# Kernel tuning notes

Measured on AMD Instinct MI355X. Metric: run time of the kernel, lower is better.

The kernel has to match this reference:

```python
import jax, jax.numpy as jnp
import numpy as np

B, S, H = 2, 4096, 2048
NH, NKV, HD = 16, 4, 128          # heads, kv heads, head_dim = H // NH
GS_RATIO = 0.25                    # hardcoded in MyAttention.forward
ROPE_BASE = 10000.0


def rotate_half(x):
    h = x.shape[-1] // 2
    return jnp.concatenate((-x[..., h:], x[..., :h]), axis=-1)


def setup_inputs() -> dict:
    key = jax.random.key(0)
    ks = jax.random.split(key, 5)
    g = int(S * GS_RATIO)
    hidden_states = jax.random.normal(ks[0], (B, S, H), jnp.float32)
    position_ids = jnp.tile(jnp.arange(S, dtype=jnp.int32)[None, :], (B, 1))
    # causal additive mask per group window (0 keep, -1e9 masked)
    i = jnp.arange(g)
    causal = i[None, :] <= i[:, None]
    attention_mask = jnp.broadcast_to(
        jnp.where(causal, 0.0, -1e9).astype(jnp.float32)[None, None], (B, 1, g, g)
    )
    sc = 0.02
    Wq = (jax.random.normal(ks[1], (H, NH * HD), jnp.float32) * sc)
    Wk = (jax.random.normal(ks[2], (H, NKV * HD), jnp.float32) * sc)
    Wv = (jax.random.normal(ks[3], (H, NKV * HD), jnp.float32) * sc)
    Wo = (jax.random.normal(ks[4], (NH * HD, H), jnp.float32) * sc)
    return {"hidden_states": hidden_states, "attention_mask": attention_mask,
            "position_ids": position_ids, "Wq": Wq, "Wk": Wk, "Wv": Wv, "Wo": Wo}


def reference(hidden_states, attention_mask, position_ids, Wq, Wk, Wv, Wo):
    B_, S_, H_ = hidden_states.shape
    g = int(S_ * GS_RATIO)
    ng = S_ // g
    n_rep = NH // NKV

    # QKV projections -> (B, heads, S, HD)
    q = (hidden_states @ Wq).reshape(B_, S_, NH, HD).transpose(0, 2, 1, 3)
    k = (hidden_states @ Wk).reshape(B_, S_, NKV, HD).transpose(0, 2, 1, 3)
    v = (hidden_states @ Wv).reshape(B_, S_, NKV, HD).transpose(0, 2, 1, 3)

    # RoPE
    inv_freq = 1.0 / (ROPE_BASE ** (jnp.arange(0, HD, 2, dtype=jnp.float32) / HD))
    t = jnp.arange(S_, dtype=jnp.float32)
    emb = jnp.concatenate([jnp.outer(t, inv_freq)] * 2, axis=-1)  # (S, HD)
    cos = jnp.cos(emb)[position_ids][:, None]  # (B,1,S,HD)
    sin = jnp.sin(emb)[position_ids][:, None]
    q = q * cos + rotate_half(q) * sin
    k = k * cos + rotate_half(k) * sin

    # GQA repeat_kv
    k = jnp.repeat(k, n_rep, axis=1)
    v = jnp.repeat(v, n_rep, axis=1)

    # S2-Attn shift: roll second half of heads by -g/2 along seq, then group
    def shift(x):
        x = jnp.concatenate([x[:, :NH // 2],
                             jnp.roll(x[:, NH // 2:], -g // 2, axis=2)], axis=1)
        return x.transpose(0, 2, 1, 3).reshape(B_ * ng, g, NH, HD).transpose(0, 2, 1, 3)

    q, k, v = shift(q), shift(k), shift(v)

    attn = jnp.einsum('bhqd,bhkd->bhqk', q, k) / np.float32(np.sqrt(HD))
    mask = jnp.tile(attention_mask, (ng, 1, 1, 1))  # (B*ng,1,g,g)
    attn = attn + mask
    attn = jax.nn.softmax(attn.astype(jnp.float32), axis=-1).astype(q.dtype)

    out = jnp.einsum('bhqk,bhkd->bhqd', attn, v)  # (B*ng, NH, g, HD)
    out = out.transpose(0, 2, 1, 3).reshape(B_, S_, NH, HD)
    # undo shift for second half of heads (+g/2 along seq)
    out = jnp.concatenate([out[:, :, :NH // 2],
                           jnp.roll(out[:, :, NH // 2:], g // 2, axis=1)], axis=2)
    out = out.reshape(B_, S_, NH * HD) @ Wo
    return out
```

## Files before the change

kernel.cpp:

```cpp
#include <hip/hip_runtime.h>
#include <math.h>

typedef unsigned short u16;
typedef short bf16x8 __attribute__((ext_vector_type(8)));
typedef float f32x4 __attribute__((ext_vector_type(4)));


__device__ __forceinline__ u16 f2bf(float x) {
  union { float f; unsigned u; } c; c.f = x;
  unsigned r = (c.u + 0x7FFFu + ((c.u >> 16) & 1u)) >> 16;
  return (u16)r;
}
__device__ __forceinline__ float bf2f(u16 x) {
  union { unsigned u; float f; } c; c.u = ((unsigned)x) << 16;
  return c.f;
}

#define GLD16(gp, lp)                                                   \
  __builtin_amdgcn_global_load_lds(                                     \
      (__attribute__((address_space(1))) void*)(gp),                    \
      (__attribute__((address_space(3))) void*)(lp), 16, 0, 0)

__global__ __launch_bounds__(256) void cast_bf16_vec(
    const float* __restrict__ X, u16* __restrict__ Y) {
  const size_t i = ((size_t)blockIdx.x * 256 + threadIdx.x) * 4;
  float4 v = *(const float4*)(X + i);
  ushort4 o;
  o.x = f2bf(v.x); o.y = f2bf(v.y); o.z = f2bf(v.z); o.w = f2bf(v.w);
  *(ushort4*)(Y + i) = o;
}

__global__ __launch_bounds__(256) void wt_cast(
    const float* __restrict__ W, u16* __restrict__ Wt, int K, int N) {
  const int bk = blockIdx.y * 64;
  const int bn = blockIdx.x * 64;
  __shared__ float T[64 * 65];
  const int tid = threadIdx.x;
  #pragma unroll
  for (int u = 0; u < 16; ++u) {
    int idx = tid + u * 256;
    int kl = idx >> 6, nl = idx & 63;
    T[kl * 65 + nl] = W[(size_t)(bk + kl) * N + bn + nl];
  }
  __syncthreads();
  #pragma unroll
  for (int u = 0; u < 16; ++u) {
    int idx = tid + u * 256;
    int nl = idx >> 6, kl = idx & 63;
    Wt[(size_t)(bn + nl) * K + bk + kl] = f2bf(T[kl * 65 + nl]);
  }
}

__global__ __launch_bounds__(512) void gemm_bf16_256(
    const u16* __restrict__ A, const u16* __restrict__ Bt,
    float* __restrict__ Cf, u16* __restrict__ Cb, int M, int N, int K) {
  __shared__ u16 As[4][256 * 32];
  __shared__ u16 Bs[4][256 * 32];

  const int tid = threadIdx.x;

  const int gridN = N >> 8;
  const int nwg = gridDim.x * gridDim.y;
  const int orig = blockIdx.y * gridDim.x + blockIdx.x;
  const int q8 = nwg >> 3, r8 = nwg & 7;
  const int xcd = orig & 7, lid = orig >> 3;
  const int wgid = (xcd < r8 ? xcd * (q8 + 1) : r8 * (q8 + 1) + (xcd - r8) * q8) + lid;
  const int bm = (wgid / gridN) << 8;
  const int bn = (wgid % gridN) << 8;

  const int w = tid >> 6, lane = tid & 63;
  const int col = lane & 15, quad = lane >> 4;
  const int wm = w >> 2, wn = w & 3;
  const int sw = (col >> 1) & 3;

  const int srow = tid >> 2;
  const int scp  = tid & 3;
  const int sc   = scp ^ ((srow >> 1) & 3);

  const u16* Ag = A  + (size_t)bm * K;
  const u16* Bg = Bt + (size_t)bn * K;
  const u16* aS0 = Ag + (size_t)srow * K + sc * 8;
  const u16* aS1 = Ag + (size_t)(srow + 128) * K + sc * 8;
  const u16* bS0 = Bg + (size_t)srow * K + sc * 8;
  const u16* bS1 = Bg + (size_t)(srow + 128) * K + sc * 8;
  const int ldst0 = srow * 32 + scp * 8;
  const int ldst1 = (srow + 128) * 32 + scp * 8;

#define STAGE_A(t, buf) { GLD16(aS0 + (size_t)(t) * 32, &As[buf][ldst0]); \
                          GLD16(aS1 + (size_t)(t) * 32, &As[buf][ldst1]); }
#define STAGE_B(t, buf) { GLD16(bS0 + (size_t)(t) * 32, &Bs[buf][ldst0]); \
                          GLD16(bS1 + (size_t)(t) * 32, &Bs[buf][ldst1]); }

  f32x4 acc[8][4];
  #pragma unroll
  for (int i = 0; i < 8; ++i)
    #pragma unroll
    for (int j = 0; j < 4; ++j) acc[i][j] = (f32x4)(0.0f);

  const int NT = K >> 5;

  STAGE_A(0, 0); STAGE_B(0, 0);
  if (NT > 1) {
    STAGE_A(1, 1); STAGE_B(1, 1);
    asm volatile("s_waitcnt vmcnt(4)" ::: "memory");
  } else {
    asm volatile("s_waitcnt vmcnt(0)" ::: "memory");
  }
  __builtin_amdgcn_s_barrier();
  asm volatile("" ::: "memory");

  const int aoff = (wm * 128 + col) * 32 + (quad ^ sw) * 8;
  const int boff = (wn * 64  + col) * 32 + (quad ^ sw) * 8;

  for (int t = 0; t < NT; ++t) {
    const int cur = t & 3;
    const bool pf = (t + 2 < NT);
    const int pbuf = (t + 2) & 3;

    bf16x8 af[4], bfr[4];
    #pragma unroll
    for (int i = 0; i < 4; ++i)
      af[i] = *(const bf16x8*)&As[cur][aoff + (16 * i) * 32];
    #pragma unroll
    for (int j = 0; j < 4; ++j)
      bfr[j] = *(const bf16x8*)&Bs[cur][boff + (16 * j) * 32];
    if (pf) STAGE_A(t + 2, pbuf);
    __builtin_amdgcn_s_barrier();
    asm volatile("s_waitcnt lgkmcnt(0)");
    __builtin_amdgcn_s_setprio(1);
    #pragma unroll
    for (int i = 0; i < 4; ++i)
      #pragma unroll
      for (int j = 0; j < 4; ++j)
        acc[i][j] = __builtin_amdgcn_mfma_f32_16x16x32_bf16(af[i], bfr[j], acc[i][j], 0, 0, 0);
    __builtin_amdgcn_s_setprio(0);
    __builtin_amdgcn_s_barrier();

    bf16x8 af2[4];
    #pragma unroll
    for (int i = 0; i < 4; ++i)
      af2[i] = *(const bf16x8*)&As[cur][aoff + ((64 + 16 * i)) * 32];
    if (pf) STAGE_B(t + 2, pbuf);
    __builtin_amdgcn_s_barrier();
    asm volatile("s_waitcnt lgkmcnt(0)");
    __builtin_amdgcn_s_setprio(1);
    #pragma unroll
    for (int i = 0; i < 4; ++i)
      #pragma unroll
      for (int j = 0; j < 4; ++j)
        acc[4 + i][j] = __builtin_amdgcn_mfma_f32_16x16x32_bf16(af2[i], bfr[j], acc[4 + i][j], 0, 0, 0);
    __builtin_amdgcn_s_setprio(0);

    if (pf) asm volatile("s_waitcnt vmcnt(4)" ::: "memory");
    else    asm volatile("s_waitcnt vmcnt(0)" ::: "memory");
    __builtin_amdgcn_s_barrier();
    asm volatile("" ::: "memory");
  }

  const int crow0 = bm + wm * 128 + quad * 4;
  const int ccol0 = bn + wn * 64 + col;
  #pragma unroll
  for (int i = 0; i < 8; ++i) {
    const int row0 = crow0 + 16 * i;
    #pragma unroll
    for (int j = 0; j < 4; ++j) {
      const int cc = ccol0 + 16 * j;
      #pragma unroll
      for (int r = 0; r < 4; ++r) {
        if (Cb) Cb[(size_t)(row0 + r) * N + cc] = f2bf(acc[i][j][r]);
        else    Cf[(size_t)(row0 + r) * N + cc] = acc[i][j][r];
      }
    }
  }
#undef STAGE_A
#undef STAGE_B
}

__global__ __launch_bounds__(256) void rope_qkv(
    u16* __restrict__ QKV, const int* __restrict__ pos) {
  const unsigned idx = blockIdx.x * 256 + threadIdx.x;
  const int d = idx & 63;
  const unsigned rest = idx >> 6;
  const int hh = rest % 20;
  const unsigned bs = rest / 20;

  const int colbase = (hh < 16) ? hh * 128 : 2048 + (hh - 16) * 128;
  u16* p = QKV + (size_t)bs * 3072 + colbase + d;
  const float x0 = bf2f(p[0]);
  const float x1 = bf2f(p[64]);
  const float t = (float)pos[bs];
  const float inv_freq = __expf((float)d * -0.14391156509676332f);
  float s, c;
  __sincosf(t * inv_freq, &s, &c);
  const float sc = (hh < 16) ? 0.08838834764831845f : 1.0f;
  p[0]  = f2bf((x0 * c - x1 * s) * sc);
  p[64] = f2bf((x1 * c + x0 * s) * sc);
}

__global__ __launch_bounds__(256) void v_transpose(
    const u16* __restrict__ QKV, u16* __restrict__ Vt) {
  const int bid = blockIdx.x;
  const int st = bid & 63;
  const int kvh = (bid >> 6) & 3;
  const int b = bid >> 8;
  __shared__ u16 T[64 * 136];
  const int tid = threadIdx.x;
  #pragma unroll
  for (int u = 0; u < 4; ++u) {
    int idx = tid + u * 256;
    int sl = idx >> 4, ch = idx & 15;
    *(uint4*)&T[sl * 136 + ch * 8] =
        *(const uint4*)(QKV + ((size_t)(b * 4096 + st * 64 + sl)) * 3072 + 2560 + kvh * 128 + ch * 8);
  }
  __syncthreads();
  #pragma unroll
  for (int u = 0; u < 32; ++u) {
    int idx = tid + u * 256;
    int d = idx >> 6, sl = idx & 63;
    Vt[((size_t)((b * 4 + kvh) * 128 + d)) * 4096 + st * 64 + sl] = T[sl * 136 + d];
  }
}

__global__ __launch_bounds__(256) void attn_mfma(
    const u16* __restrict__ QKV, const u16* __restrict__ Vt,
    u16* __restrict__ Ob) {
  __shared__ u16 Ks[64 * 136];
  __shared__ u16 Vs[128 * 72];
  __shared__ u16 Ps[4][16 * 72];

  const int bid = blockIdx.x;
  const int qt = 15 - (bid & 15);
  const int h  = (bid >> 4) & 15;
  const int gi = (bid >> 8) & 3;
  const int b  = bid >> 10;

  const int tid = threadIdx.x;
  const int w = tid >> 6, lane = tid & 63;
  const int col = lane & 15, quad = lane >> 4;

  const int shift = (h >= 8) ? 512 : 0;
  const int base_s = gi * 1024;
  const int kvh = h >> 2;

  const int sq0 = (base_s + qt * 64 + shift) & 4095;
  {
    const u16* qsrc = QKV + ((size_t)(b * 4096 + sq0)) * 3072 + h * 128;
    #pragma unroll
    for (int u = 0; u < 4; ++u) {
      int idx = tid + u * 256;
      int row = idx >> 4, ch = idx & 15;
      *(uint4*)&Ks[row * 136 + ch * 8] =
          *(const uint4*)(qsrc + (size_t)row * 3072 + ch * 8);
    }
  }
  __syncthreads();
  bf16x8 aq[4];
  #pragma unroll
  for (int kk = 0; kk < 4; ++kk)
    aq[kk] = *(const bf16x8*)&Ks[(w * 16 + col) * 136 + kk * 32 + quad * 8];

  f32x4 o[8];
  #pragma unroll
  for (int jd = 0; jd < 8; ++jd) o[jd] = (f32x4)(0.0f);
  float lp[4] = {0.0f, 0.0f, 0.0f, 0.0f};

  u16* Pw = &Ps[w][0];
  const int qrow_l = w * 16 + quad * 4;

  for (int kt = 0; kt <= qt; ++kt) {
    const int sk0 = (base_s + kt * 64 + shift) & 4095;
    __syncthreads();
    {
      const u16* ksrc = QKV + ((size_t)(b * 4096 + sk0)) * 3072 + 2048 + kvh * 128;
      #pragma unroll
      for (int u = 0; u < 4; ++u) {
        int idx = tid + u * 256;
        int row = idx >> 4, ch = idx & 15;
        *(uint4*)&Ks[row * 136 + ch * 8] =
            *(const uint4*)(ksrc + (size_t)row * 3072 + ch * 8);
      }
      const u16* vsrc = Vt + ((size_t)((b * 4 + kvh) * 128)) * 4096 + sk0;
      #pragma unroll
      for (int u = 0; u < 4; ++u) {
        int idx = tid + u * 256;
        int d = idx >> 3, ch = idx & 7;
        *(uint4*)&Vs[d * 72 + ch * 8] =
            *(const uint4*)(vsrc + (size_t)d * 4096 + ch * 8);
      }
    }
    __syncthreads();

    f32x4 sc[4];
    #pragma unroll
    for (int j = 0; j < 4; ++j) sc[j] = (f32x4)(0.0f);
    #pragma unroll
    for (int kk = 0; kk < 4; ++kk) {
      #pragma unroll
      for (int j = 0; j < 4; ++j) {
        bf16x8 bk = *(const bf16x8*)&Ks[(16 * j + col) * 136 + kk * 32 + quad * 8];
        sc[j] = __builtin_amdgcn_mfma_f32_16x16x32_bf16(aq[kk], bk, sc[j], 0, 0, 0);
      }
    }

    #pragma unroll
    for (int j = 0; j < 4; ++j) {
      #pragma unroll
      for (int r = 0; r < 4; ++r) {
        float p = __expf(sc[j][r]);
        if (kt == qt && (16 * j + col) > (qrow_l + r)) p = 0.0f;
        lp[r] += p;
        Pw[(quad * 4 + r) * 72 + 16 * j + col] = f2bf(p);
      }
    }

    #pragma unroll
    for (int ks = 0; ks < 2; ++ks) {
      bf16x8 ap = *(const bf16x8*)&Pw[col * 72 + ks * 32 + quad * 8];
      #pragma unroll
      for (int jd = 0; jd < 8; ++jd) {
        bf16x8 bv = *(const bf16x8*)&Vs[(16 * jd + col) * 72 + ks * 32 + quad * 8];
        o[jd] = __builtin_amdgcn_mfma_f32_16x16x32_bf16(ap, bv, o[jd], 0, 0, 0);
      }
    }
  }

  #pragma unroll
  for (int r = 0; r < 4; ++r) {
    lp[r] += __shfl_xor(lp[r], 1, 64);
    lp[r] += __shfl_xor(lp[r], 2, 64);
    lp[r] += __shfl_xor(lp[r], 4, 64);
    lp[r] += __shfl_xor(lp[r], 8, 64);
  }

  #pragma unroll
  for (int r = 0; r < 4; ++r) {
    const int qg = qt * 64 + w * 16 + quad * 4 + r;
    const int sq = (base_s + qg + shift) & 4095;
    u16* dst = Ob + ((size_t)(b * 4096 + sq)) * 2048 + h * 128;
    const float inv = 1.0f / lp[r];
    #pragma unroll
    for (int jd = 0; jd < 8; ++jd)
      dst[16 * jd + col] = f2bf(o[jd][r] * inv);
  }
}

extern "C" void kernel_launch(void* const* d_in, const int* in_sizes, int n_in,
                              void* d_out, int out_size, void* d_ws, size_t ws_size,
                              hipStream_t stream) {
  const float* hs = (const float*)d_in[0];
  const int*   pos = (const int*)d_in[2];
  const float* Wq = (const float*)d_in[3];
  const float* Wk = (const float*)d_in[4];
  const float* Wv = (const float*)d_in[5];
  const float* Wo = (const float*)d_in[6];

  char* ws = (char*)d_ws;
  u16* hsb   = (u16*)ws; ws += (size_t)8192 * 2048 * 2;
  u16* Wqkvt = (u16*)ws; ws += (size_t)3072 * 2048 * 2;
  u16* Wot   = (u16*)ws; ws += (size_t)2048 * 2048 * 2;
  u16* QKVb  = (u16*)ws; ws += (size_t)8192 * 3072 * 2;
  u16* Vtt   = (u16*)ws; ws += (size_t)2 * 4 * 128 * 4096 * 2;
  u16* Obh   = (u16*)ws; ws += (size_t)8192 * 2048 * 2;

  dim3 blk(256);

  cast_bf16_vec<<<16384, blk, 0, stream>>>(hs, hsb);
  wt_cast<<<dim3(32, 32), blk, 0, stream>>>(Wq, Wqkvt, 2048, 2048);
  wt_cast<<<dim3(8, 32),  blk, 0, stream>>>(Wk, Wqkvt + (size_t)2048 * 2048, 2048, 512);
  wt_cast<<<dim3(8, 32),  blk, 0, stream>>>(Wv, Wqkvt + (size_t)2560 * 2048, 2048, 512);
  wt_cast<<<dim3(32, 32), blk, 0, stream>>>(Wo, Wot, 2048, 2048);

  gemm_bf16_256<<<dim3(12, 32), dim3(512), 0, stream>>>(hsb, Wqkvt, nullptr, QKVb, 8192, 3072, 2048);

  rope_qkv<<<40960, blk, 0, stream>>>(QKVb, pos);

  v_transpose<<<512, blk, 0, stream>>>(QKVb, Vtt);

  attn_mfma<<<2048, blk, 0, stream>>>(QKVb, Vtt, Obh);

  gemm_bf16_256<<<dim3(8, 32), dim3(512), 0, stream>>>(Obh, Wot, (float*)d_out, nullptr, 8192, 2048, 2048);
}
```

Baseline: 517.2 us.

## Double-buffer K/V tiles in attention with async global-to-LDS loads and XOR swizzle

The attention kernel now uses two LDS buffers for K and V and issues direct global-to-LDS loads for the next tile before computing on the current one, with explicit vmcnt waits and barriers. The padded LDS layout is replaced by an XOR-swizzled unpadded layout to avoid bank conflicts, and MFMA sections are wrapped in s_setprio. The aim is to hide global load latency behind compute, at the cost of doubled LDS use, which may lower occupancy.

```diff
diff --git a/kernel.cpp b/kernel.cpp
--- a/kernel.cpp
+++ b/kernel.cpp
@@ -224,8 +224,8 @@
 __global__ __launch_bounds__(256) void attn_mfma(
     const u16* __restrict__ QKV, const u16* __restrict__ Vt,
     u16* __restrict__ Ob) {
-  __shared__ u16 Ks[64 * 136];
-  __shared__ u16 Vs[128 * 72];
+  __shared__ u16 Ks[2][64 * 128];
+  __shared__ u16 Vs[2][128 * 64];
   __shared__ u16 Ps[4][16 * 72];
 
   const int bid = blockIdx.x;
@@ -242,22 +242,54 @@
   const int base_s = gi * 1024;
   const int kvh = h >> 2;
 
+  const int kco8 = ((tid & 15) ^ ((tid >> 4) & 7)) << 3;
+  const int vco8 = ((tid & 7) ^ ((tid >> 3) & 7)) << 3;
+  const size_t krow = (size_t)(tid >> 4) * 3072 + kco8;
+  const size_t vrow = (size_t)(tid >> 3) * 4096 + vco8;
+  u16* kdst = &Ks[0][0] + tid * 8;
+  u16* vdst = &Vs[0][0] + tid * 8;
+  const size_t vbase = (size_t)((b * 4 + kvh) * 128) * 4096;
+  const u16* kgb = QKV + (size_t)b * 4096 * 3072 + 2048 + kvh * 128;
+
+#define ASTAGE(kt_, buf_) {                                               \
+    const int sk_ = (base_s + (kt_) * 64 + shift) & 4095;                 \
+    const u16* ks_ = kgb + (size_t)sk_ * 3072;                            \
+    const u16* vs_ = Vt + vbase + sk_;                                    \
+    GLD16(ks_ + krow,             kdst + (buf_) * 8192);                  \
+    GLD16(ks_ + krow + 16 * 3072, kdst + (buf_) * 8192 + 2048);           \
+    GLD16(ks_ + krow + 32 * 3072, kdst + (buf_) * 8192 + 4096);           \
+    GLD16(ks_ + krow + 48 * 3072, kdst + (buf_) * 8192 + 6144);           \
+    GLD16(vs_ + vrow,             vdst + (buf_) * 8192);                  \
+    GLD16(vs_ + vrow + 32 * 4096, vdst + (buf_) * 8192 + 2048);           \
+    GLD16(vs_ + vrow + 64 * 4096, vdst + (buf_) * 8192 + 4096);           \
+    GLD16(vs_ + vrow + 96 * 4096, vdst + (buf_) * 8192 + 6144);           \
+  }
+
   const int sq0 = (base_s + qt * 64 + shift) & 4095;
   {
     const u16* qsrc = QKV + ((size_t)(b * 4096 + sq0)) * 3072 + h * 128;
-    #pragma unroll
-    for (int u = 0; u < 4; ++u) {
-      int idx = tid + u * 256;
-      int row = idx >> 4, ch = idx & 15;
-      *(uint4*)&Ks[row * 136 + ch * 8] =
-          *(const uint4*)(qsrc + (size_t)row * 3072 + ch * 8);
-    }
-  }
-  __syncthreads();
+    GLD16(qsrc + krow,             kdst);
+    GLD16(qsrc + krow + 16 * 3072, kdst + 2048);
+    GLD16(qsrc + krow + 32 * 3072, kdst + 4096);
+    GLD16(qsrc + krow + 48 * 3072, kdst + 6144);
+  }
+  asm volatile("s_waitcnt vmcnt(0)" ::: "memory");
+  __builtin_amdgcn_s_barrier();
+  asm volatile("" ::: "memory");
+
+  const int cxor = col & 7;
   bf16x8 aq[4];
-  #pragma unroll
-  for (int kk = 0; kk < 4; ++kk)
-    aq[kk] = *(const bf16x8*)&Ks[(w * 16 + col) * 136 + kk * 32 + quad * 8];
+  {
+    const int qr = w * 16 + col;
+    #pragma unroll
+    for (int kk = 0; kk < 4; ++kk)
+      aq[kk] = *(const bf16x8*)&Ks[0][qr * 128 + ((((kk << 2) + quad) ^ cxor) << 3)];
+  }
+  asm volatile("s_waitcnt lgkmcnt(0)" ::: "memory");
+  __builtin_amdgcn_s_barrier();
+  asm volatile("" ::: "memory");
+
+  ASTAGE(0, 0);
 
   f32x4 o[8];
   #pragma unroll
@@ -268,61 +300,57 @@
   const int qrow_l = w * 16 + quad * 4;
 
   for (int kt = 0; kt <= qt; ++kt) {
-    const int sk0 = (base_s + kt * 64 + shift) & 4095;
-    __syncthreads();
-    {
-      const u16* ksrc = QKV + ((size_t)(b * 4096 + sk0)) * 3072 + 2048 + kvh * 128;
-      #pragma unroll
-      for (int u = 0; u < 4; ++u) {
-        int idx = tid + u * 256;
-        int row = idx >> 4, ch = idx & 15;
-        *(uint4*)&Ks[row * 136 + ch * 8] =
-            *(const uint4*)(ksrc + (size_t)row * 3072 + ch * 8);
-      }
-      const u16* vsrc = Vt + ((size_t)((b * 4 + kvh) * 128)) * 4096 + sk0;
-      #pragma unroll
-      for (int u = 0; u < 4; ++u) {
-        int idx = tid + u * 256;
-        int d = idx >> 3, ch = idx & 7;
-        *(uint4*)&Vs[d * 72 + ch * 8] =
-            *(const uint4*)(vsrc + (size_t)d * 4096 + ch * 8);
+    const u16* Kc = &Ks[kt & 1][0];
+    const u16* Vc = &Vs[kt & 1][0];
+    const bool pf = (kt < qt);
+    if (pf) ASTAGE(kt + 1, (kt + 1) & 1);
+    if (pf) asm volatile("s_waitcnt vmcnt(8)" ::: "memory");
+    else    asm volatile("s_waitcnt vmcnt(0)" ::: "memory");
+    __builtin_amdgcn_s_barrier();
+    asm volatile("" ::: "memory");
+
+    f32x4 scv[4];
+    #pragma unroll
+    for (int j = 0; j < 4; ++j) scv[j] = (f32x4)(0.0f);
+    __builtin_amdgcn_s_setprio(1);
+    #pragma unroll
+    for (int kk = 0; kk < 4; ++kk) {
+      #pragma unroll
+      for (int j = 0; j < 4; ++j) {
+        bf16x8 bk = *(const bf16x8*)&Kc[(16 * j + col) * 128 + ((((kk << 2) + quad) ^ cxor) << 3)];
+        scv[j] = __builtin_amdgcn_mfma_f32_16x16x32_bf16(aq[kk], bk, scv[j], 0, 0, 0);
       }
     }
-    __syncthreads();
-
-    f32x4 sc[4];
-    #pragma unroll
-    for (int j = 0; j < 4; ++j) sc[j] = (f32x4)(0.0f);
-    #pragma unroll
-    for (int kk = 0; kk < 4; ++kk) {
-      #pragma unroll
-      for (int j = 0; j < 4; ++j) {
-        bf16x8 bk = *(const bf16x8*)&Ks[(16 * j + col) * 136 + kk * 32 + quad * 8];
-        sc[j] = __builtin_amdgcn_mfma_f32_16x16x32_bf16(aq[kk], bk, sc[j], 0, 0, 0);
-      }
-    }
-
+    __builtin_amdgcn_s_setprio(0);
+
+    const bool last = (kt == qt);
     #pragma unroll
     for (int j = 0; j < 4; ++j) {
       #pragma unroll
       for (int r = 0; r < 4; ++r) {
-        float p = __expf(sc[j][r]);
-        if (kt == qt && (16 * j + col) > (qrow_l + r)) p = 0.0f;
+        float p = __expf(scv[j][r]);
+        if (last && (16 * j + col) > (qrow_l + r)) p = 0.0f;
         lp[r] += p;
         Pw[(quad * 4 + r) * 72 + 16 * j + col] = f2bf(p);
       }
     }
 
+    __builtin_amdgcn_s_setprio(1);
     #pragma unroll
     for (int ks = 0; ks < 2; ++ks) {
       bf16x8 ap = *(const bf16x8*)&Pw[col * 72 + ks * 32 + quad * 8];
       #pragma unroll
       for (int jd = 0; jd < 8; ++jd) {
-        bf16x8 bv = *(const bf16x8*)&Vs[(16 * jd + col) * 72 + ks * 32 + quad * 8];
+        bf16x8 bv = *(const bf16x8*)&Vc[(16 * jd + col) * 64 + ((((ks << 2) + quad) ^ cxor) << 3)];
         o[jd] = __builtin_amdgcn_mfma_f32_16x16x32_bf16(ap, bv, o[jd], 0, 0, 0);
       }
     }
-  }
+    __builtin_amdgcn_s_setprio(0);
+
+    asm volatile("" ::: "memory");
+    __builtin_amdgcn_s_barrier();
+  }
+#undef ASTAGE
 
   #pragma unroll
   for (int r = 0; r < 4; ++r) {
```

Result: faster. 502.6 us (-2.8%).
